# Kernel tuning notes

Measured on AMD Instinct MI355X. Metric: run time of the kernel, lower is better.

The kernel has to match this reference:

```python
import jax, jax.numpy as jnp
import numpy as np

LN_EPS = 1e-5


def _ln(x, g, b):
    mu = jnp.mean(x, -1, keepdims=True)
    xc = x - mu
    inv = jax.lax.rsqrt(jnp.mean(xc * xc, -1, keepdims=True) + LN_EPS)
    return xc * inv * g + b


def _subm_conv(x, nbr, W, b):
    # Submanifold 3D conv via rulebook gather-GEMM-accumulate.
    # x: [N, Cin], nbr: [N, K] neighbor row ids (-1 = missing), W: [K, Cin, Cout], b: [Cout]
    N = x.shape[0]
    xp = jnp.concatenate([x, jnp.zeros((1, x.shape[1]), x.dtype)], 0)  # sentinel zero row
    idx = jnp.where(nbr < 0, N, nbr)  # missing neighbors -> zero row
    acc0 = jnp.zeros((N, W.shape[-1]), x.dtype) + b
    def body(acc, xs):
        i, Wk = xs  # i: [N], Wk: [Cin, Cout]
        return acc + xp[i] @ Wk, None
    acc, _ = jax.lax.scan(body, acc0, (idx.T, W))
    return acc


def _blk1(x, W, b, g, be):  # 1x1x1 SubMConv + LN + ReLU
    return jax.nn.relu(_ln(x @ W + b, g, be))


def _blk3(x, nbr, W, b, g, be):  # 3x3x3 SubMConv + LN + ReLU
    return jax.nn.relu(_ln(_subm_conv(x, nbr, W, b), g, be))


def setup_inputs() -> dict:
    rng = np.random.default_rng(0)
    B, D, Npb, K = 2, 160, 131072, 27
    dim, half = 64, 32
    # Build random sparse voxel set and the rulebook (neighbor table) like spconv does.
    lookup = np.full((B, D, D, D), -1, np.int64)
    coords = np.zeros((B * Npb, 3), np.int64)
    for b in range(B):
        lin = np.sort(rng.choice(D * D * D, size=Npb, replace=False))
        z, y, x = np.unravel_index(lin, (D, D, D))
        rows = np.arange(b * Npb, (b + 1) * Npb)
        lookup[b, z, y, x] = rows
        coords[rows] = np.stack([z, y, x], 1)
    bidx = np.repeat(np.arange(B), Npb)
    offs = np.stack(np.meshgrid(np.arange(-1, 2), np.arange(-1, 2), np.arange(-1, 2), indexing="ij"), -1).reshape(K, 3)
    nz = coords[:, None, :] + offs[None]  # [N, K, 3]
    valid = ((nz >= 0) & (nz < D)).all(-1)
    nzc = np.clip(nz, 0, D - 1)
    nbr = lookup[bidx[:, None], nzc[..., 0], nzc[..., 1], nzc[..., 2]]
    nbr = np.where(valid, nbr, -1).astype(np.int32)

    key = jax.random.key(0)
    ks = iter(jax.random.split(key, 16))
    f32 = jnp.float32
    d = {"voxel_features": jax.random.normal(next(ks), (B * Npb, dim), f32),
         "nbr_idx": jnp.asarray(nbr)}
    def lnp(c):
        return jnp.ones((c,), f32), jnp.zeros((c,), f32)
    d["W1"] = 0.05 * jax.random.normal(next(ks), (dim, dim), f32); d["b1"] = jnp.zeros((dim,), f32); d["g1"], d["be1"] = lnp(dim)
    d["W2"] = 0.05 * jax.random.normal(next(ks), (dim, dim), f32); d["b2"] = jnp.zeros((dim,), f32); d["g2"], d["be2"] = lnp(dim)
    d["W3"] = 0.05 * jax.random.normal(next(ks), (K, dim, half), f32); d["b3"] = jnp.zeros((half,), f32); d["g3"], d["be3"] = lnp(half)
    d["W4"] = 0.05 * jax.random.normal(next(ks), (K, half, half), f32); d["b4"] = jnp.zeros((half,), f32); d["g4"], d["be4"] = lnp(half)
    d["W5"] = 0.05 * jax.random.normal(next(ks), (K, half, half), f32); d["b5"] = jnp.zeros((half,), f32); d["g5"], d["be5"] = lnp(half)
    d["W6"] = 0.05 * jax.random.normal(next(ks), (K, half, half), f32); d["b6"] = jnp.zeros((half,), f32); d["g6"], d["be6"] = lnp(half)
    d["W7"] = 0.05 * jax.random.normal(next(ks), (4 * dim, dim), f32); d["b7"] = jnp.zeros((dim,), f32); d["g7"], d["be7"] = lnp(dim)
    return d


def reference(voxel_features, nbr_idx,
              W1, b1, g1, be1, W2, b2, g2, be2,
              W3, b3, g3, be3, W4, b4, g4, be4,
              W5, b5, g5, be5, W6, b6, g6, be6,
              W7, b7, g7, be7):
    x = voxel_features
    f1 = _blk1(x, W1, b1, g1, be1)
    f2 = _blk1(x, W2, b2, g2, be2)
    feats = [f1, f2]
    f2 = _blk3(f2, nbr_idx, W3, b3, g3, be3); feats.append(f2)
    f2 = _blk3(f2, nbr_idx, W4, b4, g4, be4); feats.append(f2)
    f2 = _blk3(f2, nbr_idx, W5, b5, g5, be5); feats.append(f2)
    f2 = _blk3(f2, nbr_idx, W6, b6, g6, be6); feats.append(f2)
    cat = jnp.concatenate(feats, -1)  # [N, 4*dim]
    return _blk1(cat, W7, b7, g7, be7)
```

## Files before the change

### kernel.cpp

```cpp
#include <hip/hip_runtime.h>

typedef __attribute__((ext_vector_type(4))) float  float4_;
typedef __attribute__((ext_vector_type(8))) short  short8;
typedef __attribute__((ext_vector_type(8))) __bf16 bf16x8;

__device__ inline unsigned short f2bf(float f) {
    unsigned u = __builtin_bit_cast(unsigned, f);
    u += 0x7FFFu + ((u >> 16) & 1u);
    return (unsigned short)(u >> 16);
}

__device__ inline float4_ mfma16(bf16x8 a, bf16x8 b, float4_ c) {
    return __builtin_amdgcn_mfma_f32_16x16x32_bf16(a, b, c, 0, 0, 0);
}


__global__ void packW_kernel(const float* __restrict__ src, unsigned short* __restrict__ dst,
                             int cin, int cout, int total) {
    int e = blockIdx.x * 256 + threadIdx.x;
    if (e >= total) return;
    int f = e >> 9, i = e & 511, lane = i >> 3, t = i & 7;
    int ntn = cout >> 4, ctn = cin >> 5;
    int nt = f % ntn;
    int rest = f / ntn;
    int ct = rest % ctn;
    int k = rest / ctn;
    int c = ct * 32 + (lane >> 4) * 8 + t;
    int j = nt * 16 + (lane & 15);
    dst[e] = f2bf(src[(k * cin + c) * cout + j]);
}

__global__ void pack2_kernel(const float* __restrict__ W1, const float* __restrict__ W2,
                             unsigned short* __restrict__ dst) {
    int e = blockIdx.x * 256 + threadIdx.x;
    if (e >= 8192) return;
    int f = e >> 9, i = e & 511, lane = i >> 3, t = i & 7;
    int nt = f & 7, ct = f >> 3;
    int c = ct * 32 + (lane >> 4) * 8 + t;
    int j = nt * 16 + (lane & 15);
    float v = (j < 64) ? W1[c * 64 + j] : W2[c * 64 + (j - 64)];
    dst[e] = f2bf(v);
}

__global__ void zero_row_kernel(unsigned short* cat, int N) {
    ((unsigned*)(cat + (size_t)N * 256))[threadIdx.x] = 0;
}

__global__ __launch_bounds__(256) void blk12_kernel(
    const float* __restrict__ x, unsigned short* cat,
    const unsigned short* __restrict__ Wp,
    const float* __restrict__ b1, const float* __restrict__ g1, const float* __restrict__ be1,
    const float* __restrict__ b2, const float* __restrict__ g2, const float* __restrict__ be2) {
    int tid = threadIdx.x, lane = tid & 63, wv = tid >> 6;
    int l15 = lane & 15, q = lane >> 4;
    long base = ((long)blockIdx.x * 4 + wv) * 16;

    float4_ acc[8];
#pragma unroll
    for (int i = 0; i < 8; i++) acc[i] = (float4_){0.f, 0.f, 0.f, 0.f};

#pragma unroll
    for (int kt = 0; kt < 2; kt++) {
        const float* xp = x + (base + l15) * 64 + kt * 32 + q * 8;
        float4_ f0 = *(const float4_*)xp;
        float4_ f1 = *(const float4_*)(xp + 4);
        short8 as;
        as[0] = (short)f2bf(f0[0]); as[1] = (short)f2bf(f0[1]);
        as[2] = (short)f2bf(f0[2]); as[3] = (short)f2bf(f0[3]);
        as[4] = (short)f2bf(f1[0]); as[5] = (short)f2bf(f1[1]);
        as[6] = (short)f2bf(f1[2]); as[7] = (short)f2bf(f1[3]);
        bf16x8 a = __builtin_bit_cast(bf16x8, as);
        const unsigned short* wp = Wp + (size_t)kt * 8 * 512;
#pragma unroll
        for (int nt = 0; nt < 8; nt++) {
            bf16x8 w = *(const bf16x8*)(wp + nt * 512 + lane * 8);
            acc[nt] = mfma16(a, w, acc[nt]);
        }
    }

    float bc[8], gc[8], bec[8];
#pragma unroll
    for (int nt = 0; nt < 8; nt++) {
        int j = nt * 16 + l15;
        if (j < 64) { bc[nt] = b1[j]; gc[nt] = g1[j]; bec[nt] = be1[j]; }
        else        { bc[nt] = b2[j - 64]; gc[nt] = g2[j - 64]; bec[nt] = be2[j - 64]; }
    }

#pragma unroll
    for (int r = 0; r < 4; r++) {
        long row = base + q * 4 + r;
        float v[8], s0 = 0.f, s1 = 0.f, q0 = 0.f, q1 = 0.f;
#pragma unroll
        for (int nt = 0; nt < 4; nt++) { v[nt] = acc[nt][r] + bc[nt]; s0 += v[nt]; q0 += v[nt] * v[nt]; }
#pragma unroll
        for (int nt = 4; nt < 8; nt++) { v[nt] = acc[nt][r] + bc[nt]; s1 += v[nt]; q1 += v[nt] * v[nt]; }
#pragma unroll
        for (int m = 1; m < 16; m <<= 1) {
            s0 += __shfl_xor(s0, m); q0 += __shfl_xor(q0, m);
            s1 += __shfl_xor(s1, m); q1 += __shfl_xor(q1, m);
        }
        float mu0 = s0 * (1.f / 64), var0 = q0 * (1.f / 64) - mu0 * mu0, inv0 = rsqrtf(var0 + 1e-5f);
        float mu1 = s1 * (1.f / 64), var1 = q1 * (1.f / 64) - mu1 * mu1, inv1 = rsqrtf(var1 + 1e-5f);
        unsigned short* cp = cat + row * 256;
#pragma unroll
        for (int nt = 0; nt < 4; nt++) {
            float y = fmaxf((v[nt] - mu0) * inv0 * gc[nt] + bec[nt], 0.f);
            cp[nt * 16 + l15] = f2bf(y);
        }
#pragma unroll
        for (int nt = 4; nt < 8; nt++) {
            float y = fmaxf((v[nt] - mu1) * inv1 * gc[nt] + bec[nt], 0.f);
            cp[nt * 16 + l15] = f2bf(y);
        }
    }
}

template <int CT, int MT>
__global__ __launch_bounds__(256) void conv_kernel(
    unsigned short* cat, const int* __restrict__ nbr,
    const unsigned short* __restrict__ Wp,
    const float* __restrict__ bb, const float* __restrict__ gg, const float* __restrict__ bee,
    int in_off, int out_off, int N) {
    int tid = threadIdx.x, lane = tid & 63, wv = tid >> 6;
    int l15 = lane & 15, q = lane >> 4;
    long base = ((long)blockIdx.x * 4 + wv) * (MT * 16);

    float4_ acc[MT][2];
#pragma unroll
    for (int mt = 0; mt < MT; mt++) {
        acc[mt][0] = (float4_){0.f, 0.f, 0.f, 0.f};
        acc[mt][1] = (float4_){0.f, 0.f, 0.f, 0.f};
    }

    const unsigned short* catp = cat + in_off + q * 8;
    const int* nbp[MT];
#pragma unroll
    for (int mt = 0; mt < MT; mt++) nbp[mt] = nbr + (base + mt * 16 + l15) * 27;

    int idxn[MT];
    bf16x8 a[MT][CT], b[MT][CT];
#pragma unroll
    for (int mt = 0; mt < MT; mt++) {
        int v = nbp[mt][0];
        int ic = v < 0 ? N : v;
#pragma unroll
        for (int ct = 0; ct < CT; ct++)
            a[mt][ct] = *(const bf16x8*)(catp + (size_t)ic * 256 + ct * 32);
    }
#pragma unroll
    for (int mt = 0; mt < MT; mt++) {
        int v = nbp[mt][1];
        idxn[mt] = v < 0 ? N : v;
    }

    const unsigned short* wp = Wp + lane * 8;
    for (int k = 0; k < 27; k++) {
        int k2 = (k + 2 < 27) ? k + 2 : 26;
        int idx2[MT];
#pragma unroll
        for (int mt = 0; mt < MT; mt++) {
            int v = nbp[mt][k2];
            idx2[mt] = v < 0 ? N : v;
        }
#pragma unroll
        for (int mt = 0; mt < MT; mt++)
#pragma unroll
            for (int ct = 0; ct < CT; ct++)
                b[mt][ct] = *(const bf16x8*)(catp + (size_t)idxn[mt] * 256 + ct * 32);
#pragma unroll
        for (int ct = 0; ct < CT; ct++) {
            bf16x8 w0 = *(const bf16x8*)(wp + ct * 1024);
            bf16x8 w1 = *(const bf16x8*)(wp + ct * 1024 + 512);
#pragma unroll
            for (int mt = 0; mt < MT; mt++) {
                acc[mt][0] = mfma16(a[mt][ct], w0, acc[mt][0]);
                acc[mt][1] = mfma16(a[mt][ct], w1, acc[mt][1]);
            }
        }
        wp += CT * 1024;
#pragma unroll
        for (int mt = 0; mt < MT; mt++) {
#pragma unroll
            for (int ct = 0; ct < CT; ct++) a[mt][ct] = b[mt][ct];
            idxn[mt] = idx2[mt];
        }
    }

    float b0c = bb[l15], b1c = bb[16 + l15];
    float g0c = gg[l15], g1c = gg[16 + l15];
    float be0c = bee[l15], be1c = bee[16 + l15];

#pragma unroll
    for (int mt = 0; mt < MT; mt++) {
#pragma unroll
        for (int r = 0; r < 4; r++) {
            long row = base + mt * 16 + q * 4 + r;
            float v0 = acc[mt][0][r] + b0c;
            float v1 = acc[mt][1][r] + b1c;
            float s = v0 + v1, sq = v0 * v0 + v1 * v1;
#pragma unroll
            for (int m = 1; m < 16; m <<= 1) { s += __shfl_xor(s, m); sq += __shfl_xor(sq, m); }
            float mu = s * (1.f / 32), var = sq * (1.f / 32) - mu * mu, inv = rsqrtf(var + 1e-5f);
            float y0 = fmaxf((v0 - mu) * inv * g0c + be0c, 0.f);
            float y1 = fmaxf((v1 - mu) * inv * g1c + be1c, 0.f);
            unsigned short* cp = cat + row * 256 + out_off;
            cp[l15] = f2bf(y0);
            cp[16 + l15] = f2bf(y1);
        }
    }
}

__global__ __launch_bounds__(256) void blk7_kernel(
    const unsigned short* __restrict__ cat, const unsigned short* __restrict__ Wp,
    const float* __restrict__ b, const float* __restrict__ g, const float* __restrict__ be,
    float* __restrict__ out) {
    int tid = threadIdx.x, lane = tid & 63, wv = tid >> 6;
    int l15 = lane & 15, q = lane >> 4;
    long base = ((long)blockIdx.x * 4 + wv) * 16;

    float4_ acc[4];
#pragma unroll
    for (int i = 0; i < 4; i++) acc[i] = (float4_){0.f, 0.f, 0.f, 0.f};

#pragma unroll
    for (int kt = 0; kt < 8; kt++) {
        bf16x8 a = *(const bf16x8*)(cat + (base + l15) * 256 + kt * 32 + q * 8);
        const unsigned short* wp = Wp + (size_t)kt * 4 * 512;
#pragma unroll
        for (int nt = 0; nt < 4; nt++) {
            bf16x8 w = *(const bf16x8*)(wp + nt * 512 + lane * 8);
            acc[nt] = mfma16(a, w, acc[nt]);
        }
    }

    float bc[4], gc[4], bec[4];
#pragma unroll
    for (int nt = 0; nt < 4; nt++) {
        int j = nt * 16 + l15;
        bc[nt] = b[j]; gc[nt] = g[j]; bec[nt] = be[j];
    }

#pragma unroll
    for (int r = 0; r < 4; r++) {
        long row = base + q * 4 + r;
        float v[4], s = 0.f, sq = 0.f;
#pragma unroll
        for (int nt = 0; nt < 4; nt++) { v[nt] = acc[nt][r] + bc[nt]; s += v[nt]; sq += v[nt] * v[nt]; }
#pragma unroll
        for (int m = 1; m < 16; m <<= 1) { s += __shfl_xor(s, m); sq += __shfl_xor(sq, m); }
        float mu = s * (1.f / 64), var = sq * (1.f / 64) - mu * mu, inv = rsqrtf(var + 1e-5f);
#pragma unroll
        for (int nt = 0; nt < 4; nt++) {
            float y = fmaxf((v[nt] - mu) * inv * gc[nt] + bec[nt], 0.f);
            out[row * 64 + nt * 16 + l15] = y;
        }
    }
}

extern "C" void kernel_launch(void* const* d_in, const int* in_sizes, int n_in,
                              void* d_out, int out_size, void* d_ws, size_t ws_size,
                              hipStream_t stream) {
    const int N = in_sizes[0] / 64;

    const float* x   = (const float*)d_in[0];
    const int*   nbr = (const int*)d_in[1];
    const float* W1 = (const float*)d_in[2];
    const float* b1 = (const float*)d_in[3];
    const float* g1 = (const float*)d_in[4];
    const float* be1 = (const float*)d_in[5];
    const float* W2 = (const float*)d_in[6];
    const float* b2 = (const float*)d_in[7];
    const float* g2 = (const float*)d_in[8];
    const float* be2 = (const float*)d_in[9];
    const float* W3 = (const float*)d_in[10];
    const float* b3 = (const float*)d_in[11];
    const float* g3 = (const float*)d_in[12];
    const float* be3 = (const float*)d_in[13];
    const float* W4 = (const float*)d_in[14];
    const float* b4 = (const float*)d_in[15];
    const float* g4 = (const float*)d_in[16];
    const float* be4 = (const float*)d_in[17];
    const float* W5 = (const float*)d_in[18];
    const float* b5 = (const float*)d_in[19];
    const float* g5 = (const float*)d_in[20];
    const float* be5 = (const float*)d_in[21];
    const float* W6 = (const float*)d_in[22];
    const float* b6 = (const float*)d_in[23];
    const float* g6 = (const float*)d_in[24];
    const float* be6 = (const float*)d_in[25];
    const float* W7 = (const float*)d_in[26];
    const float* b7 = (const float*)d_in[27];
    const float* g7 = (const float*)d_in[28];
    const float* be7 = (const float*)d_in[29];

    unsigned short* ws   = (unsigned short*)d_ws;
    unsigned short* cat  = ws;
    unsigned short* Wp12 = cat + (size_t)(N + 1) * 256;
    unsigned short* Wp3  = Wp12 + 8192;
    unsigned short* Wp4  = Wp3 + 55296;
    unsigned short* Wp5  = Wp4 + 27648;
    unsigned short* Wp6  = Wp5 + 27648;
    unsigned short* Wp7  = Wp6 + 27648;

    zero_row_kernel<<<1, 128, 0, stream>>>(cat, N);
    pack2_kernel<<<32, 256, 0, stream>>>(W1, W2, Wp12);
    packW_kernel<<<(55296 + 255) / 256, 256, 0, stream>>>(W3, Wp3, 64, 32, 55296);
    packW_kernel<<<(27648 + 255) / 256, 256, 0, stream>>>(W4, Wp4, 32, 32, 27648);
    packW_kernel<<<(27648 + 255) / 256, 256, 0, stream>>>(W5, Wp5, 32, 32, 27648);
    packW_kernel<<<(27648 + 255) / 256, 256, 0, stream>>>(W6, Wp6, 32, 32, 27648);
    packW_kernel<<<(16384 + 255) / 256, 256, 0, stream>>>(W7, Wp7, 256, 64, 16384);

    blk12_kernel<<<N / 64, 256, 0, stream>>>(x, cat, Wp12, b1, g1, be1, b2, g2, be2);
    conv_kernel<2, 2><<<N / 128, 256, 0, stream>>>(cat, nbr, Wp3, b3, g3, be3, 64, 128, N);
    conv_kernel<1, 4><<<N / 256, 256, 0, stream>>>(cat, nbr, Wp4, b4, g4, be4, 128, 160, N);
    conv_kernel<1, 4><<<N / 256, 256, 0, stream>>>(cat, nbr, Wp5, b5, g5, be5, 160, 192, N);
    conv_kernel<1, 4><<<N / 256, 256, 0, stream>>>(cat, nbr, Wp6, b6, g6, be6, 192, 224, N);
    blk7_kernel<<<N / 64, 256, 0, stream>>>(cat, Wp7, b7, g7, be7, (float*)d_out);
}
```

Before: 509.5 us.

## Deepen gather prefetch pipeline in sparse conv and merge weight-packing launches

The conv kernel is rewritten to keep a ring of D+1 gathered feature tiles in flight, prefetch the packed weights two taps ahead into registers, and fully unroll the 27-tap loop. Rows per wave are fixed at 32 (MT=2), which doubles the grid for the 32-channel layers. This is meant to hide gather latency. The seven weight-pack and zero-row launches are merged into one kernel to cut launch overhead. The cost is much higher register pressure from the deeper buffers and full unroll, which may lower occupancy.

```diff
diff --git a/kernel.cpp b/kernel.cpp
--- a/kernel.cpp
+++ b/kernel.cpp
@@ -14,11 +14,8 @@
     return __builtin_amdgcn_mfma_f32_16x16x32_bf16(a, b, c, 0, 0, 0);
 }
 
-
-__global__ void packW_kernel(const float* __restrict__ src, unsigned short* __restrict__ dst,
-                             int cin, int cout, int total) {
-    int e = blockIdx.x * 256 + threadIdx.x;
-    if (e >= total) return;
+__device__ inline void packW_one(const float* __restrict__ src, unsigned short* __restrict__ dst,
+                                 int cin, int cout, int e) {
     int f = e >> 9, i = e & 511, lane = i >> 3, t = i & 7;
     int ntn = cout >> 4, ctn = cin >> 5;
     int nt = f % ntn;
@@ -30,20 +27,36 @@
     dst[e] = f2bf(src[(k * cin + c) * cout + j]);
 }
 
-__global__ void pack2_kernel(const float* __restrict__ W1, const float* __restrict__ W2,
-                             unsigned short* __restrict__ dst) {
+__global__ void pack_all_kernel(
+    const float* __restrict__ W1, const float* __restrict__ W2,
+    const float* __restrict__ W3, const float* __restrict__ W4,
+    const float* __restrict__ W5, const float* __restrict__ W6,
+    const float* __restrict__ W7,
+    unsigned short* cat, unsigned short* Wp12, unsigned short* Wp3,
+    unsigned short* Wp4, unsigned short* Wp5, unsigned short* Wp6,
+    unsigned short* Wp7, int N) {
     int e = blockIdx.x * 256 + threadIdx.x;
-    if (e >= 8192) return;
-    int f = e >> 9, i = e & 511, lane = i >> 3, t = i & 7;
-    int nt = f & 7, ct = f >> 3;
-    int c = ct * 32 + (lane >> 4) * 8 + t;
-    int j = nt * 16 + (lane & 15);
-    float v = (j < 64) ? W1[c * 64 + j] : W2[c * 64 + (j - 64)];
-    dst[e] = f2bf(v);
-}
-
-__global__ void zero_row_kernel(unsigned short* cat, int N) {
-    ((unsigned*)(cat + (size_t)N * 256))[threadIdx.x] = 0;
+    if (e < 8192) {
+        int f = e >> 9, i = e & 511, lane = i >> 3, t = i & 7;
+        int nt = f & 7, ct = f >> 3;
+        int c = ct * 32 + (lane >> 4) * 8 + t;
+        int j = nt * 16 + (lane & 15);
+        float v = (j < 64) ? W1[c * 64 + j] : W2[c * 64 + (j - 64)];
+        Wp12[e] = f2bf(v);
+        return;
+    }
+    e -= 8192;
+    if (e < 55296) { packW_one(W3, Wp3, 64, 32, e); return; }
+    e -= 55296;
+    if (e < 27648) { packW_one(W4, Wp4, 32, 32, e); return; }
+    e -= 27648;
+    if (e < 27648) { packW_one(W5, Wp5, 32, 32, e); return; }
+    e -= 27648;
+    if (e < 27648) { packW_one(W6, Wp6, 32, 32, e); return; }
+    e -= 27648;
+    if (e < 16384) { packW_one(W7, Wp7, 256, 64, e); return; }
+    e -= 16384;
+    if (e < 128) ((unsigned*)(cat + (size_t)N * 256))[e] = 0;
 }
 
 __global__ __launch_bounds__(256) void blk12_kernel(
@@ -115,15 +128,16 @@
     }
 }
 
-template <int CT, int MT>
+template <int CT, int D>
 __global__ __launch_bounds__(256) void conv_kernel(
     unsigned short* cat, const int* __restrict__ nbr,
     const unsigned short* __restrict__ Wp,
     const float* __restrict__ bb, const float* __restrict__ gg, const float* __restrict__ bee,
     int in_off, int out_off, int N) {
+    const int MT = 2;
     int tid = threadIdx.x, lane = tid & 63, wv = tid >> 6;
     int l15 = lane & 15, q = lane >> 4;
-    long base = ((long)blockIdx.x * 4 + wv) * (MT * 16);
+    long base = ((long)blockIdx.x * 4 + wv) * 32;
 
     float4_ acc[MT][2];
 #pragma unroll
@@ -133,56 +147,78 @@
     }
 
     const unsigned short* catp = cat + in_off + q * 8;
+    const unsigned short* wl = Wp + lane * 8;
     const int* nbp[MT];
 #pragma unroll
     for (int mt = 0; mt < MT; mt++) nbp[mt] = nbr + (base + mt * 16 + l15) * 27;
 
-    int idxn[MT];
-    bf16x8 a[MT][CT], b[MT][CT];
+    bf16x8 f[D + 1][MT][CT];
+    bf16x8 wr[3][CT][2];
+    int rawi[3][MT];
+
+    int raw0[D + 2][MT];
+#pragma unroll
+    for (int j = 0; j < D + 2; j++)
+#pragma unroll
+        for (int mt = 0; mt < MT; mt++) raw0[j][mt] = nbp[mt][j];
+
+#pragma unroll
+    for (int kk = 0; kk < 2; kk++)
+#pragma unroll
+        for (int ct = 0; ct < CT; ct++)
+#pragma unroll
+            for (int nt = 0; nt < 2; nt++)
+                wr[kk][ct][nt] = *(const bf16x8*)(wl + ((size_t)((kk * CT + ct) * 2 + nt)) * 512);
+
+#pragma unroll
+    for (int j = 0; j < D; j++)
+#pragma unroll
+        for (int mt = 0; mt < MT; mt++) {
+            int v = raw0[j][mt];
+            size_t s = (size_t)(v < 0 ? N : v);
+#pragma unroll
+            for (int ct = 0; ct < CT; ct++)
+                f[j][mt][ct] = *(const bf16x8*)(catp + s * 256 + ct * 32);
+        }
 #pragma unroll
     for (int mt = 0; mt < MT; mt++) {
-        int v = nbp[mt][0];
-        int ic = v < 0 ? N : v;
-#pragma unroll
-        for (int ct = 0; ct < CT; ct++)
-            a[mt][ct] = *(const bf16x8*)(catp + (size_t)ic * 256 + ct * 32);
-    }
-#pragma unroll
-    for (int mt = 0; mt < MT; mt++) {
-        int v = nbp[mt][1];
-        idxn[mt] = v < 0 ? N : v;
-    }
-
-    const unsigned short* wp = Wp + lane * 8;
+        rawi[D % 3][mt] = raw0[D][mt];
+        rawi[(D + 1) % 3][mt] = raw0[D + 1][mt];
+    }
+
+#pragma unroll
     for (int k = 0; k < 27; k++) {
-        int k2 = (k + 2 < 27) ? k + 2 : 26;
-        int idx2[MT];
-#pragma unroll
-        for (int mt = 0; mt < MT; mt++) {
-            int v = nbp[mt][k2];
-            idx2[mt] = v < 0 ? N : v;
-        }
-#pragma unroll
-        for (int mt = 0; mt < MT; mt++)
+        if (k + 2 < 27) {
 #pragma unroll
             for (int ct = 0; ct < CT; ct++)
-                b[mt][ct] = *(const bf16x8*)(catp + (size_t)idxn[mt] * 256 + ct * 32);
+#pragma unroll
+                for (int nt = 0; nt < 2; nt++)
+                    wr[(k + 2) % 3][ct][nt] =
+                        *(const bf16x8*)(wl + ((size_t)(((k + 2) * CT + ct) * 2 + nt)) * 512);
+        }
+        if (k + D < 27) {
+#pragma unroll
+            for (int mt = 0; mt < MT; mt++) {
+                int v = rawi[(k + D) % 3][mt];
+                size_t s = (size_t)(v < 0 ? N : v);
+#pragma unroll
+                for (int ct = 0; ct < CT; ct++)
+                    f[(k + D) % (D + 1)][mt][ct] = *(const bf16x8*)(catp + s * 256 + ct * 32);
+            }
+        }
+        if (k + D + 2 < 27) {
+#pragma unroll
+            for (int mt = 0; mt < MT; mt++) rawi[(k + D + 2) % 3][mt] = nbp[mt][k + D + 2];
+        }
 #pragma unroll
         for (int ct = 0; ct < CT; ct++) {
-            bf16x8 w0 = *(const bf16x8*)(wp + ct * 1024);
-            bf16x8 w1 = *(const bf16x8*)(wp + ct * 1024 + 512);
+            bf16x8 w0 = wr[k % 3][ct][0];
+            bf16x8 w1 = wr[k % 3][ct][1];
 #pragma unroll
             for (int mt = 0; mt < MT; mt++) {
-                acc[mt][0] = mfma16(a[mt][ct], w0, acc[mt][0]);
-                acc[mt][1] = mfma16(a[mt][ct], w1, acc[mt][1]);
+                acc[mt][0] = mfma16(f[k % (D + 1)][mt][ct], w0, acc[mt][0]);
+                acc[mt][1] = mfma16(f[k % (D + 1)][mt][ct], w1, acc[mt][1]);
             }
-        }
-        wp += CT * 1024;
-#pragma unroll
-        for (int mt = 0; mt < MT; mt++) {
-#pragma unroll
-            for (int ct = 0; ct < CT; ct++) a[mt][ct] = b[mt][ct];
-            idxn[mt] = idx2[mt];
         }
     }
 
@@ -302,18 +338,13 @@
     unsigned short* Wp6  = Wp5 + 27648;
     unsigned short* Wp7  = Wp6 + 27648;
 
-    zero_row_kernel<<<1, 128, 0, stream>>>(cat, N);
-    pack2_kernel<<<32, 256, 0, stream>>>(W1, W2, Wp12);
-    packW_kernel<<<(55296 + 255) / 256, 256, 0, stream>>>(W3, Wp3, 64, 32, 55296);
-    packW_kernel<<<(27648 + 255) / 256, 256, 0, stream>>>(W4, Wp4, 32, 32, 27648);
-    packW_kernel<<<(27648 + 255) / 256, 256, 0, stream>>>(W5, Wp5, 32, 32, 27648);
-    packW_kernel<<<(27648 + 255) / 256, 256, 0, stream>>>(W6, Wp6, 32, 32, 27648);
-    packW_kernel<<<(16384 + 255) / 256, 256, 0, stream>>>(W7, Wp7, 256, 64, 16384);
+    pack_all_kernel<<<637, 256, 0, stream>>>(W1, W2, W3, W4, W5, W6, W7,
+                                             cat, Wp12, Wp3, Wp4, Wp5, Wp6, Wp7, N);
 
     blk12_kernel<<<N / 64, 256, 0, stream>>>(x, cat, Wp12, b1, g1, be1, b2, g2, be2);
-    conv_kernel<2, 2><<<N / 128, 256, 0, stream>>>(cat, nbr, Wp3, b3, g3, be3, 64, 128, N);
-    conv_kernel<1, 4><<<N / 256, 256, 0, stream>>>(cat, nbr, Wp4, b4, g4, be4, 128, 160, N);
-    conv_kernel<1, 4><<<N / 256, 256, 0, stream>>>(cat, nbr, Wp5, b5, g5, be5, 160, 192, N);
-    conv_kernel<1, 4><<<N / 256, 256, 0, stream>>>(cat, nbr, Wp6, b6, g6, be6, 192, 224, N);
+    conv_kernel<2, 3><<<N / 128, 256, 0, stream>>>(cat, nbr, Wp3, b3, g3, be3, 64, 128, N);
+    conv_kernel<1, 4><<<N / 128, 256, 0, stream>>>(cat, nbr, Wp4, b4, g4, be4, 128, 160, N);
+    conv_kernel<1, 4><<<N / 128, 256, 0, stream>>>(cat, nbr, Wp5, b5, g5, be5, 160, 192, N);
+    conv_kernel<1, 4><<<N / 128, 256, 0, stream>>>(cat, nbr, Wp6, b6, g6, be6, 192, 224, N);
     blk7_kernel<<<N / 64, 256, 0, stream>>>(cat, Wp7, b7, g7, be7, (float*)d_out);
 }
```

New measurement: 441.4 us. -13.4%, faster.
